# Kernel tuning notes

Measured on AMD Instinct MI355X. Metric: run time of the kernel, lower is better.

Reference implementation:

```python
import jax, jax.numpy as jnp
import numpy as np

PATCH = 3          # patch size for SSD cost
PAD = PATCH // 2
K_NN = 8           # number of NN candidates kept per pixel
N_ITERS = 10       # PatchMatch iterations (forward default n_iters=10)
_DY = jnp.array([d // PATCH for d in range(PATCH * PATCH)], dtype=jnp.int32)
_DX = jnp.array([d % PATCH for d in range(PATCH * PATCH)], dtype=jnp.int32)


def _patches(x):
    # x: [C,H,W] -> [C, P*P, H, W] edge-padded patch neighborhoods
    C, H, W = x.shape
    xp = jnp.pad(x, ((0, 0), (PAD, PAD), (PAD, PAD)), mode='edge')
    return jnp.stack([xp[:, dy:dy + H, dx:dx + W]
                      for dy in range(PATCH) for dx in range(PATCH)], axis=1)


def _cost(a_pat, b_pad, s):
    # a_pat: [C,P2,H,W]; b_pad: [C,H+2p,W+2p]; s: [2,H,W] int -> SSD cost [H,W]
    iy = s[0][None] + _DY[:, None, None]   # [P2,H,W]
    ix = s[1][None] + _DX[:, None, None]
    b_g = b_pad[:, iy, ix]                 # [C,P2,H,W] gathered target patches
    return jnp.sum((a_pat - b_g) ** 2, axis=(0, 1))


def patchmatch_search(a, b, key, k=K_NN, n_iters=N_ITERS):
    # a, b: [C,H,W]. Returns shifts [k,2,H,W] int32 and costs [k,H,W].
    C, H, W = a.shape
    a_pat = _patches(a)
    b_pad = jnp.pad(b, ((0, 0), (PAD, PAD), (PAD, PAD)), mode='edge')
    cost1 = lambda s: _cost(a_pat, b_pad, s)
    hi = jnp.array([H, W], dtype=jnp.int32).reshape(1, 2, 1, 1)
    dx1 = jnp.array([0, 1], jnp.int32).reshape(1, 2, 1, 1)
    dy1 = jnp.array([1, 0], jnp.int32).reshape(1, 2, 1, 1)
    k0, key = jax.random.split(key)
    shifts = jax.random.randint(k0, (k, 2, H, W), 0, hi)
    costs = jax.lax.map(cost1, shifts)
    radii = [max(W // 2, 1), max(W // 8, 1), max(W // 32, 1), 1]

    def step(carry, it):
        shifts, costs = carry
        kk = jax.random.fold_in(key, it)
        # parallel propagation of neighbors' shifts
        left = jnp.roll(shifts, 1, axis=3) + dx1
        right = jnp.roll(shifts, -1, axis=3) - dx1
        up = jnp.roll(shifts, 1, axis=2) + dy1
        down = jnp.roll(shifts, -1, axis=2) - dy1
        # random search with shrinking radii
        rand_c = [shifts + jax.random.randint(jax.random.fold_in(kk, i),
                                              shifts.shape, -r, r + 1)
                  for i, r in enumerate(radii)]
        cands = jnp.concatenate([left, right, up, down] + rand_c, axis=0)
        cands = jnp.clip(cands, 0, hi - 1)
        new_costs = jax.lax.map(cost1, cands)
        all_s = jnp.concatenate([shifts, cands], axis=0)      # [M,2,H,W]
        all_c = jnp.concatenate([costs, new_costs], axis=0)   # [M,H,W]
        neg_top, idx = jax.lax.top_k(-jnp.moveaxis(all_c, 0, -1), k)  # [H,W,k]
        s_hw = jnp.transpose(all_s, (2, 3, 0, 1))             # [H,W,M,2]
        sel = jnp.take_along_axis(s_hw, idx[..., None], axis=2)  # [H,W,k,2]
        return (jnp.transpose(sel, (2, 3, 0, 1)), jnp.moveaxis(-neg_top, -1, 0)), None

    (shifts, costs), _ = jax.lax.scan(step, (shifts, costs), jnp.arange(n_iters))
    return shifts, costs


def setup_inputs() -> dict:
    key = jax.random.key(0)
    kq, kk, kv = jax.random.split(key, 3)
    q = jax.random.normal(kq, (1, 32, 128, 128), jnp.float32)
    k = jax.random.normal(kk, (1, 32, 128, 128), jnp.float32)
    v = jax.random.normal(kv, (4, 64, 128, 128), jnp.float32)
    return {"q": q, "k": k, "v": v}


def reference(q, k, v):
    # PatchMatch k-NN search between q[0] and k[0]
    shifts, costs = patchmatch_search(q[0], k[0], jax.random.key(42))
    w = jax.nn.softmax(-costs, axis=0)                 # [K,H,W]
    g = v[:, :, shifts[:, 0], shifts[:, 1]]            # [B,Cv,K,H,W] gather
    return jnp.sum(w[None, None] * g, axis=2)          # [B,Cv,H,W]
```

## Files before the change

### kernel.cpp

```cpp
#include <hip/hip_runtime.h>
#include <cstdint>

#define NPIX 16384
#define KNN 8
#define PW 130
#define NPPAD (PW * PW)
#define LSTR 19

typedef float f32x4 __attribute__((ext_vector_type(4)));

__host__ __device__ __forceinline__ void tf2x32(uint32_t k0, uint32_t k1,
                                                uint32_t x0, uint32_t x1,
                                                uint32_t& o0, uint32_t& o1) {
  uint32_t ks2 = k0 ^ k1 ^ 0x1BD11BDAu;
  x0 += k0; x1 += k1;
#define TFR(r) { x0 += x1; x1 = (x1 << r) | (x1 >> (32 - r)); x1 ^= x0; }
  TFR(13) TFR(15) TFR(26) TFR(6)  x0 += k1;  x1 += ks2 + 1u;
  TFR(17) TFR(29) TFR(16) TFR(24) x0 += ks2; x1 += k0 + 2u;
  TFR(13) TFR(15) TFR(26) TFR(6)  x0 += k0;  x1 += k1 + 3u;
  TFR(17) TFR(29) TFR(16) TFR(24) x0 += k1;  x1 += ks2 + 4u;
  TFR(13) TFR(15) TFR(26) TFR(6)  x0 += ks2; x1 += k0 + 5u;
#undef TFR
  o0 = x0; o1 = x1;
}

__device__ __forceinline__ uint32_t rbits32(uint32_t ka, uint32_t kb, uint32_t j) {
  uint32_t o0, o1;
  tf2x32(ka, kb, 0u, j, o0, o1);
  return o0 ^ o1;
}

__device__ __forceinline__ int rnd_int(uint4 K, uint32_t j, uint32_t span,
                                       uint32_t mult, int minv) {
  uint32_t hi = rbits32(K.x, K.y, j);
  uint32_t lo = rbits32(K.z, K.w, j);
  uint32_t off = ((hi % span) * mult + (lo % span)) % span;
  return minv + (int)off;
}

__device__ __forceinline__ float cost_eval_pl(const float* __restrict__ apt,
                                              const float* __restrict__ bpt,
                                              int py0, int px0, int sy, int sx) {
  float acc = 0.f;
#pragma unroll
  for (int ph = 0; ph < 4; ++ph) {
    const float* ab = apt + ((size_t)ph * NPPAD + (size_t)(py0 * PW + px0)) * 8;
    const float* bb = bpt + ((size_t)ph * NPPAD + (size_t)(sy * PW + sx)) * 8;
#pragma unroll
    for (int ccq = 0; ccq < 2; ++ccq) {
      f32x4 av[9], bv[9];
#pragma unroll
      for (int p = 0; p < 9; ++p) {
        int dy = p / 3, dx = p - dy * 3;
        av[p] = *(const f32x4*)(ab + (dy * PW + dx) * 8 + ccq * 4);
        bv[p] = *(const f32x4*)(bb + (dy * PW + dx) * 8 + ccq * 4);
      }
#pragma unroll
      for (int j = 0; j < 4; ++j) {
#pragma unroll
        for (int p = 0; p < 9; ++p) {
          float d = __fsub_rn(av[p][j], bv[p][j]);
          acc = __fadd_rn(acc, __fmul_rn(d, d));
        }
      }
    }
  }
  return acc;
}

__global__ __launch_bounds__(256) void pad_kernel(
    const float* __restrict__ a, const float* __restrict__ b,
    float* __restrict__ apt, float* __restrict__ bpt) {
  int t = (int)(blockIdx.x * blockDim.x + threadIdx.x);
  if (t >= 4 * NPPAD * 8) return;
  int lo = t & 7;
  int rest = t >> 3;
  int pos = rest % NPPAD;
  int ph = rest / NPPAD;
  int c = ph * 8 + lo;
  int py = pos / PW, px = pos % PW;
  int y = py - 1; y = y < 0 ? 0 : (y > 127 ? 127 : y);
  int x = px - 1; x = x < 0 ? 0 : (x > 127 ? 127 : x);
  int src = (c << 14) + (y << 7) + x;
  apt[t] = a[src];
  bpt[t] = b[src];
}

__global__ __launch_bounds__(256) void init_kernel(
    const float* __restrict__ apt, const float* __restrict__ bpt,
    uint32_t* __restrict__ npack, float* __restrict__ ncost, uint4 IK) {
  int t = (int)(blockIdx.x * blockDim.x + threadIdx.x);
  int pix = t & (NPIX - 1);
  int s = t >> 14;
  int py0 = pix >> 7, px0 = pix & 127;
  uint32_t j0 = (uint32_t)(s * 2) * 16384u + (uint32_t)pix;
  int sy = rnd_int(IK, j0, 128u, 0u, 0);
  int sx = rnd_int(IK, j0 + 16384u, 128u, 0u, 0);
  float cst = cost_eval_pl(apt, bpt, py0, px0, sy, sx);
  npack[t] = (uint32_t)((sy << 7) | sx);
  ncost[t] = cst;
}

__global__ __launch_bounds__(64, 2) void step_kernel(
    const float* __restrict__ apt, const float* __restrict__ bpt,
    const uint32_t* __restrict__ ppack, const float* __restrict__ pcost,
    uint32_t* __restrict__ npack, float* __restrict__ ncost,
    uint4 K0, uint4 K1, uint4 K2, uint4 K3) {
  __shared__ f32x4 lds[64 * LSTR];
  int bidx = (int)blockIdx.x;
  int pix = ((bidx & 7) << 11) | (bidx >> 3);
  int lane = (int)threadIdx.x;
  int py0 = pix >> 7, px0 = pix & 127;
  int g = lane >> 3, s = lane & 7;

  uint32_t old_pack = 0u; float old_cost_f = 0.f;
  if (lane < 8) {
    old_pack = ppack[lane * NPIX + pix];
    old_cost_f = pcost[lane * NPIX + pix];
  }

  int sy, sx;
  if (g < 4) {
    int nh = py0, nw = px0, dsy = 0, dsx = 0;
    if (g == 0)      { nw = (px0 + 127) & 127; dsx = 1;  }
    else if (g == 1) { nw = (px0 + 1) & 127;   dsx = -1; }
    else if (g == 2) { nh = (py0 + 127) & 127; dsy = 1;  }
    else             { nh = (py0 + 1) & 127;   dsy = -1; }
    uint32_t p = ppack[s * NPIX + (nh << 7) + nw];
    sy = (int)(p >> 7) + dsy;
    sx = (int)(p & 127u) + dsx;
  } else {
    uint32_t p = ppack[s * NPIX + pix];
    uint4 Ki      = (g == 4) ? K0   : (g == 5) ? K1  : (g == 6) ? K2 : K3;
    uint32_t span = (g == 4) ? 129u : (g == 5) ? 33u : (g == 6) ? 9u : 3u;
    uint32_t mult = (g == 4) ? 16u  : (g == 5) ? 4u  : (g == 6) ? 4u : 1u;
    int minv      = (g == 4) ? -64  : (g == 5) ? -16 : (g == 6) ? -4 : -1;
    uint32_t j0 = (uint32_t)(s * 2) * 16384u + (uint32_t)pix;
    sy = (int)(p >> 7)   + rnd_int(Ki, j0, span, mult, minv);
    sx = (int)(p & 127u) + rnd_int(Ki, j0 + 16384u, span, mult, minv);
  }
  sy = sy < 0 ? 0 : (sy > 127 ? 127 : sy);
  sx = sx < 0 ? 0 : (sx > 127 ? 127 : sx);
  uint32_t cnd_pack = (uint32_t)((sy << 7) | sx);

  float acc = 0.f;
  f32x4 stg[18];

#define STAGE_LOAD(PH)                                                      \
  _Pragma("unroll")                                                         \
  for (int i = 0; i < 18; ++i) {                                            \
    int f = i * 64 + lane;                                                  \
    int c = f / 18, q = f - c * 18;                                         \
    int pos = q >> 1, ccq = q & 1;                                          \
    int dy = pos / 3, dx = pos - dy * 3;                                    \
    uint32_t pk = (uint32_t)__shfl((int)cnd_pack, c);                       \
    int py = (int)(pk >> 7) + dy;                                           \
    int px = (int)(pk & 127u) + dx;                                         \
    stg[i] = *(const f32x4*)(bpt + ((size_t)(PH) * NPPAD                    \
             + (size_t)(py * PW + px)) * 8 + ccq * 4);                      \
  }

#define STAGE_WRITE()                                                       \
  _Pragma("unroll")                                                         \
  for (int i = 0; i < 18; ++i) {                                            \
    int f = i * 64 + lane;                                                  \
    int c = f / 18, q = f - c * 18;                                         \
    lds[c * LSTR + q] = stg[i];                                             \
  }

#define EVAL(PH)                                                            \
  {                                                                         \
    const float* ab = apt + ((size_t)(PH) * NPPAD                           \
                     + (size_t)(py0 * PW + px0)) * 8;                       \
    _Pragma("unroll")                                                       \
    for (int ccq = 0; ccq < 2; ++ccq) {                                     \
      f32x4 av[9], bv[9];                                                   \
      _Pragma("unroll")                                                     \
      for (int p = 0; p < 9; ++p) {                                         \
        int dy = p / 3, dx = p - dy * 3;                                    \
        bv[p] = lds[lane * LSTR + p * 2 + ccq];                             \
        av[p] = *(const f32x4*)(ab + (dy * PW + dx) * 8 + ccq * 4);         \
      }                                                                     \
      _Pragma("unroll")                                                     \
      for (int j = 0; j < 4; ++j) {                                         \
        _Pragma("unroll")                                                   \
        for (int p = 0; p < 9; ++p) {                                       \
          float d = __fsub_rn(av[p][j], bv[p][j]);                          \
          acc = __fadd_rn(acc, __fmul_rn(d, d));                            \
        }                                                                   \
      }                                                                     \
    }                                                                       \
  }

  STAGE_LOAD(0)
  STAGE_WRITE()
  STAGE_LOAD(1)
  EVAL(0)
  STAGE_WRITE()
  STAGE_LOAD(2)
  EVAL(1)
  STAGE_WRITE()
  STAGE_LOAD(3)
  EVAL(2)
  STAGE_WRITE()
  EVAL(3)
#undef STAGE_LOAD
#undef STAGE_WRITE
#undef EVAL

  float cnd_cost = acc;

  unsigned long long new_key =
      ((unsigned long long)__float_as_uint(cnd_cost) << 32) | (unsigned)(8 + lane);
  unsigned long long old_key = (lane < 8)
      ? (((unsigned long long)__float_as_uint(old_cost_f) << 32) | (unsigned)lane)
      : ~0ull;
  bool new_used = false, old_used = (lane >= 8);

  unsigned long long wk0, wk1, wk2, wk3, wk4, wk5, wk6, wk7;
#define SELECT_ROUND(WK)                                                   \
  {                                                                        \
    unsigned long long kmin = new_used ? ~0ull : new_key;                  \
    if (!old_used && old_key < kmin) kmin = old_key;                       \
    _Pragma("unroll")                                                      \
    for (int off = 32; off; off >>= 1) {                                   \
      unsigned long long o = __shfl_xor(kmin, off);                        \
      if (o < kmin) kmin = o;                                              \
    }                                                                      \
    WK = kmin;                                                             \
    if (!new_used && new_key == kmin) new_used = true;                     \
    else if (!old_used && old_key == kmin) old_used = true;                \
  }
  SELECT_ROUND(wk0) SELECT_ROUND(wk1) SELECT_ROUND(wk2) SELECT_ROUND(wk3)
  SELECT_ROUND(wk4) SELECT_ROUND(wk5) SELECT_ROUND(wk6) SELECT_ROUND(wk7)
#undef SELECT_ROUND

  uint32_t out_pack = 0u; float out_cost = 0.f;
#define EXTRACT_ROUND(R, WK)                                               \
  {                                                                        \
    unsigned long long kmin = WK;                                          \
    uint32_t idx = (uint32_t)kmin;                                         \
    float cst = __uint_as_float((uint32_t)(kmin >> 32));                   \
    int srcOld = (idx < 8u) ? (int)idx : 0;                                \
    int srcNew = (idx >= 8u) ? (int)(idx - 8u) : 0;                        \
    uint32_t po = __shfl(old_pack, srcOld);                                \
    uint32_t pn = __shfl(cnd_pack, srcNew);                                \
    uint32_t pk = (idx < 8u) ? po : pn;                                    \
    if (lane == R) { out_pack = pk; out_cost = cst; }                      \
  }
  EXTRACT_ROUND(0, wk0) EXTRACT_ROUND(1, wk1) EXTRACT_ROUND(2, wk2)
  EXTRACT_ROUND(3, wk3) EXTRACT_ROUND(4, wk4) EXTRACT_ROUND(5, wk5)
  EXTRACT_ROUND(6, wk6) EXTRACT_ROUND(7, wk7)
#undef EXTRACT_ROUND

  if (lane < 8) {
    npack[lane * NPIX + pix] = out_pack;
    ncost[lane * NPIX + pix] = out_cost;
  }
}

__global__ __launch_bounds__(256) void weights_kernel(
    const float* __restrict__ cost0, float* __restrict__ wbuf) {
  int pix = (int)(blockIdx.x * blockDim.x + threadIdx.x);
  if (pix >= NPIX) return;
  float c[KNN];
  float m = 3.4e38f;
#pragma unroll
  for (int s = 0; s < KNN; ++s) { c[s] = cost0[s * NPIX + pix]; m = fminf(m, c[s]); }
  float e[KNN]; float sum = 0.f;
#pragma unroll
  for (int s = 0; s < KNN; ++s) { e[s] = expf(m - c[s]); sum += e[s]; }
  float inv = 1.f / sum;
#pragma unroll
  for (int s = 0; s < KNN; ++s) wbuf[s * NPIX + pix] = e[s] * inv;
}

__global__ __launch_bounds__(256) void out_kernel(
    const float* __restrict__ v, const uint32_t* __restrict__ pack0,
    const float* __restrict__ wbuf, float* __restrict__ out) {
  int t = (int)(blockIdx.x * blockDim.x + threadIdx.x);
  int pix = t & (NPIX - 1);
  int ch = t >> 14;
  const float* vc = v + ((size_t)ch << 14);
  float acc = 0.f;
#pragma unroll
  for (int s = 0; s < KNN; ++s) {
    uint32_t p = pack0[s * NPIX + pix];
    float wgt = wbuf[s * NPIX + pix];
    acc = fmaf(wgt, vc[p], acc);
  }
  out[t] = acc;
}

static void h_split_fl(uint32_t ka, uint32_t kb, uint32_t o[4]) {
  tf2x32(ka, kb, 0u, 0u, o[0], o[1]);
  tf2x32(ka, kb, 0u, 1u, o[2], o[3]);
}

extern "C" void kernel_launch(void* const* d_in, const int* in_sizes, int n_in,
                              void* d_out, int out_size, void* d_ws, size_t ws_size,
                              hipStream_t stream) {
  const float* q = (const float*)d_in[0];
  const float* k = (const float*)d_in[1];
  const float* v = (const float*)d_in[2];
  float* out = (float*)d_out;

  uint32_t* ws = (uint32_t*)d_ws;
  uint32_t* pk[2] = { ws, ws + (size_t)KNN * NPIX };
  float* ct[2] = { (float*)(ws + (size_t)2 * KNN * NPIX),
                   (float*)(ws + (size_t)3 * KNN * NPIX) };
  float* wbuf = (float*)(ws + (size_t)4 * KNN * NPIX);
  float* apt  = (float*)(ws + (size_t)5 * KNN * NPIX);
  float* bpt  = apt + (size_t)4 * NPPAD * 8;

  uint32_t sp[4];
  h_split_fl(0u, 42u, sp);
  uint32_t k0a = sp[0], k0b = sp[1];
  uint32_t kMa = sp[2], kMb = sp[3];

  pad_kernel<<<(4 * NPPAD * 8 + 255) / 256, 256, 0, stream>>>(q, k, apt, bpt);

  uint32_t ik[4];
  h_split_fl(k0a, k0b, ik);
  init_kernel<<<(KNN * NPIX) / 256, 256, 0, stream>>>(apt, bpt, pk[0], ct[0],
                                        make_uint4(ik[0], ik[1], ik[2], ik[3]));

  for (int it = 0; it < 10; ++it) {
    uint32_t ka, kb;
    tf2x32(kMa, kMb, 0u, (uint32_t)it, ka, kb);
    uint4 K[4];
    for (int i = 0; i < 4; ++i) {
      uint32_t ia, ib;
      tf2x32(ka, kb, 0u, (uint32_t)i, ia, ib);
      uint32_t o[4];
      h_split_fl(ia, ib, o);
      K[i] = make_uint4(o[0], o[1], o[2], o[3]);
    }
    step_kernel<<<NPIX, 64, 0, stream>>>(apt, bpt, pk[it & 1], ct[it & 1],
                                         pk[(it + 1) & 1], ct[(it + 1) & 1],
                                         K[0], K[1], K[2], K[3]);
  }

  weights_kernel<<<NPIX / 256, 256, 0, stream>>>(ct[0], wbuf);
  out_kernel<<<(4 * 64 * NPIX) / 256, 256, 0, stream>>>(v, pk[0], wbuf, out);
}
```

Before: 973.3 us.

## Repack padded planes to 4-channel groups, precompute gather offsets, deepen staging pipeline

Changes the padded layout from 4 planes of 8 channels to 8 planes of 4 channels, so each staging pass loads 9 float4 per lane instead of 18. Gather addresses are computed once and reused across all planes, and LDS shrinks to 576 entries with no padding stride. Launch bounds rise to 4 blocks per SIMD and compiler fences pin the order of load, eval and write. The aim is lower register pressure, higher occupancy and less per-pass address arithmetic, at the cost of twice as many pipeline stages and possible LDS bank conflicts from the stride-9 reads.

```diff
diff --git a/kernel.cpp b/kernel.cpp
--- a/kernel.cpp
+++ b/kernel.cpp
@@ -5,9 +5,10 @@
 #define KNN 8
 #define PW 130
 #define NPPAD (PW * PW)
-#define LSTR 19
 
 typedef float f32x4 __attribute__((ext_vector_type(4)));
+
+#define FENCE asm volatile("" ::: "memory");
 
 __host__ __device__ __forceinline__ void tf2x32(uint32_t k0, uint32_t k1,
                                                 uint32_t x0, uint32_t x1,
@@ -43,25 +44,22 @@
                                               int py0, int px0, int sy, int sx) {
   float acc = 0.f;
 #pragma unroll
-  for (int ph = 0; ph < 4; ++ph) {
-    const float* ab = apt + ((size_t)ph * NPPAD + (size_t)(py0 * PW + px0)) * 8;
-    const float* bb = bpt + ((size_t)ph * NPPAD + (size_t)(sy * PW + sx)) * 8;
-#pragma unroll
-    for (int ccq = 0; ccq < 2; ++ccq) {
-      f32x4 av[9], bv[9];
+  for (int ph = 0; ph < 8; ++ph) {
+    const float* ab = apt + ((size_t)ph * NPPAD + (size_t)(py0 * PW + px0)) * 4;
+    const float* bb = bpt + ((size_t)ph * NPPAD + (size_t)(sy * PW + sx)) * 4;
+    f32x4 av[9], bv[9];
+#pragma unroll
+    for (int p = 0; p < 9; ++p) {
+      int dy = p / 3, dx = p - dy * 3;
+      av[p] = *(const f32x4*)(ab + (dy * PW + dx) * 4);
+      bv[p] = *(const f32x4*)(bb + (dy * PW + dx) * 4);
+    }
+#pragma unroll
+    for (int j = 0; j < 4; ++j) {
 #pragma unroll
       for (int p = 0; p < 9; ++p) {
-        int dy = p / 3, dx = p - dy * 3;
-        av[p] = *(const f32x4*)(ab + (dy * PW + dx) * 8 + ccq * 4);
-        bv[p] = *(const f32x4*)(bb + (dy * PW + dx) * 8 + ccq * 4);
-      }
-#pragma unroll
-      for (int j = 0; j < 4; ++j) {
-#pragma unroll
-        for (int p = 0; p < 9; ++p) {
-          float d = __fsub_rn(av[p][j], bv[p][j]);
-          acc = __fadd_rn(acc, __fmul_rn(d, d));
-        }
+        float d = __fsub_rn(av[p][j], bv[p][j]);
+        acc = __fadd_rn(acc, __fmul_rn(d, d));
       }
     }
   }
@@ -72,12 +70,12 @@
     const float* __restrict__ a, const float* __restrict__ b,
     float* __restrict__ apt, float* __restrict__ bpt) {
   int t = (int)(blockIdx.x * blockDim.x + threadIdx.x);
-  if (t >= 4 * NPPAD * 8) return;
-  int lo = t & 7;
-  int rest = t >> 3;
+  if (t >= 32 * NPPAD) return;
+  int lo = t & 3;
+  int rest = t >> 2;
   int pos = rest % NPPAD;
   int ph = rest / NPPAD;
-  int c = ph * 8 + lo;
+  int c = ph * 4 + lo;
   int py = pos / PW, px = pos % PW;
   int y = py - 1; y = y < 0 ? 0 : (y > 127 ? 127 : y);
   int x = px - 1; x = x < 0 ? 0 : (x > 127 ? 127 : x);
@@ -101,12 +99,12 @@
   ncost[t] = cst;
 }
 
-__global__ __launch_bounds__(64, 2) void step_kernel(
+__global__ __launch_bounds__(64, 4) void step_kernel(
     const float* __restrict__ apt, const float* __restrict__ bpt,
     const uint32_t* __restrict__ ppack, const float* __restrict__ pcost,
     uint32_t* __restrict__ npack, float* __restrict__ ncost,
     uint4 K0, uint4 K1, uint4 K2, uint4 K3) {
-  __shared__ f32x4 lds[64 * LSTR];
+  __shared__ f32x4 lds[576];
   int bidx = (int)blockIdx.x;
   int pix = ((bidx & 7) << 11) | (bidx >> 3);
   int lane = (int)threadIdx.x;
@@ -143,51 +141,50 @@
   sx = sx < 0 ? 0 : (sx > 127 ? 127 : sx);
   uint32_t cnd_pack = (uint32_t)((sy << 7) | sx);
 
+  int base_[9];
+#pragma unroll
+  for (int i = 0; i < 9; ++i) {
+    int f = i * 64 + lane;
+    int c = f / 9, p = f - c * 9;
+    int dy = p / 3, dx = p - dy * 3;
+    uint32_t pk = (uint32_t)__shfl((int)cnd_pack, c);
+    int py = (int)(pk >> 7) + dy;
+    int px = (int)(pk & 127u) + dx;
+    base_[i] = (py * PW + px) * 4;
+  }
+
   float acc = 0.f;
-  f32x4 stg[18];
+  f32x4 stg[9];
 
 #define STAGE_LOAD(PH)                                                      \
   _Pragma("unroll")                                                         \
-  for (int i = 0; i < 18; ++i) {                                            \
-    int f = i * 64 + lane;                                                  \
-    int c = f / 18, q = f - c * 18;                                         \
-    int pos = q >> 1, ccq = q & 1;                                          \
-    int dy = pos / 3, dx = pos - dy * 3;                                    \
-    uint32_t pk = (uint32_t)__shfl((int)cnd_pack, c);                       \
-    int py = (int)(pk >> 7) + dy;                                           \
-    int px = (int)(pk & 127u) + dx;                                         \
-    stg[i] = *(const f32x4*)(bpt + ((size_t)(PH) * NPPAD                    \
-             + (size_t)(py * PW + px)) * 8 + ccq * 4);                      \
+  for (int i = 0; i < 9; ++i) {                                             \
+    stg[i] = *(const f32x4*)(bpt + (size_t)(PH) * (NPPAD * 4) + base_[i]);  \
   }
 
 #define STAGE_WRITE()                                                       \
   _Pragma("unroll")                                                         \
-  for (int i = 0; i < 18; ++i) {                                            \
-    int f = i * 64 + lane;                                                  \
-    int c = f / 18, q = f - c * 18;                                         \
-    lds[c * LSTR + q] = stg[i];                                             \
+  for (int i = 0; i < 9; ++i) {                                             \
+    lds[i * 64 + lane] = stg[i];                                            \
   }
 
 #define EVAL(PH)                                                            \
   {                                                                         \
-    const float* ab = apt + ((size_t)(PH) * NPPAD                           \
-                     + (size_t)(py0 * PW + px0)) * 8;                       \
+    const float* ab = apt + (size_t)(PH) * (NPPAD * 4)                      \
+                     + (size_t)(py0 * PW + px0) * 4;                        \
+    f32x4 av[9], bv[9];                                                     \
     _Pragma("unroll")                                                       \
-    for (int ccq = 0; ccq < 2; ++ccq) {                                     \
-      f32x4 av[9], bv[9];                                                   \
+    for (int p = 0; p < 9; ++p) {                                           \
+      int dy = p / 3, dx = p - dy * 3;                                      \
+      bv[p] = lds[lane * 9 + p];                                            \
+      av[p] = *(const f32x4*)(ab + (dy * PW + dx) * 4);                     \
+    }                                                                       \
+    _Pragma("unroll")                                                       \
+    for (int j = 0; j < 4; ++j) {                                           \
       _Pragma("unroll")                                                     \
       for (int p = 0; p < 9; ++p) {                                         \
-        int dy = p / 3, dx = p - dy * 3;                                    \
-        bv[p] = lds[lane * LSTR + p * 2 + ccq];                             \
-        av[p] = *(const f32x4*)(ab + (dy * PW + dx) * 8 + ccq * 4);         \
-      }                                                                     \
-      _Pragma("unroll")                                                     \
-      for (int j = 0; j < 4; ++j) {                                         \
-        _Pragma("unroll")                                                   \
-        for (int p = 0; p < 9; ++p) {                                       \
-          float d = __fsub_rn(av[p][j], bv[p][j]);                          \
-          acc = __fadd_rn(acc, __fmul_rn(d, d));                            \
-        }                                                                   \
+        float d = __fsub_rn(av[p][j], bv[p][j]);                            \
+        acc = __fadd_rn(acc, __fmul_rn(d, d));                              \
       }                                                                     \
     }                                                                       \
   }
@@ -195,15 +192,42 @@
   STAGE_LOAD(0)
   STAGE_WRITE()
   STAGE_LOAD(1)
+  FENCE
   EVAL(0)
+  FENCE
   STAGE_WRITE()
   STAGE_LOAD(2)
+  FENCE
   EVAL(1)
+  FENCE
   STAGE_WRITE()
   STAGE_LOAD(3)
+  FENCE
   EVAL(2)
-  STAGE_WRITE()
+  FENCE
+  STAGE_WRITE()
+  STAGE_LOAD(4)
+  FENCE
   EVAL(3)
+  FENCE
+  STAGE_WRITE()
+  STAGE_LOAD(5)
+  FENCE
+  EVAL(4)
+  FENCE
+  STAGE_WRITE()
+  STAGE_LOAD(6)
+  FENCE
+  EVAL(5)
+  FENCE
+  STAGE_WRITE()
+  STAGE_LOAD(7)
+  FENCE
+  EVAL(6)
+  FENCE
+  STAGE_WRITE()
+  FENCE
+  EVAL(7)
 #undef STAGE_LOAD
 #undef STAGE_WRITE
 #undef EVAL
@@ -311,14 +335,14 @@
                    (float*)(ws + (size_t)3 * KNN * NPIX) };
   float* wbuf = (float*)(ws + (size_t)4 * KNN * NPIX);
   float* apt  = (float*)(ws + (size_t)5 * KNN * NPIX);
-  float* bpt  = apt + (size_t)4 * NPPAD * 8;
+  float* bpt  = apt + (size_t)32 * NPPAD;
 
   uint32_t sp[4];
   h_split_fl(0u, 42u, sp);
   uint32_t k0a = sp[0], k0b = sp[1];
   uint32_t kMa = sp[2], kMb = sp[3];
 
-  pad_kernel<<<(4 * NPPAD * 8 + 255) / 256, 256, 0, stream>>>(q, k, apt, bpt);
+  pad_kernel<<<(32 * NPPAD + 255) / 256, 256, 0, stream>>>(q, k, apt, bpt);
 
   uint32_t ik[4];
   h_split_fl(k0a, k0b, ik);
```

New measurement: 915.9 us. 1.06x faster.
